# Optimization experiments

Hardware: AMD Instinct MI355X
Metric: run time of the kernel (lower is better)

Reference implementation:

```python
import jax, jax.numpy as jnp
import numpy as np

B, H, S, D = 4, 16, 2048, 64

def setup_inputs() -> dict:
    key = jax.random.key(0)
    kq, kk, kv = jax.random.split(key, 3)
    return {
        "query": jax.random.normal(kq, (B, H, S, D), dtype=jnp.float32),
        "key": jax.random.normal(kk, (B, H, S, D), dtype=jnp.float32),
        "value": jax.random.normal(kv, (B, H, S, D), dtype=jnp.float32),
        "dropout_p": 0,
    }

def reference(query, key, value, dropout_p):
    # qk: [B,H,S,S] materialized as in the original (unfused SDPA)
    scale = query.shape[-1] ** -0.5
    qk = jnp.einsum("bhqd,bhkd->bhqk", query, key) * scale
    attn = jax.nn.softmax(qk, axis=-1)
    # dropout_p == 0 -> identity (keeps reference deterministic)
    out = jnp.einsum("bhqk,bhkd->bhqd", attn, value)
    return out
```

## Files before the change

### kernel.cpp

```cpp
#include <hip/hip_runtime.h>
#include <hip/hip_bf16.h>

#define B_   4
#define H_   16
#define SEQ  2048
#define DH   64
#define BM   256
#define BN   64
#define NBH  (B_ * H_)
#define NELEM (NBH * SEQ * DH)

typedef __bf16 bf16x8 __attribute__((ext_vector_type(8)));
typedef float  f32x4  __attribute__((ext_vector_type(4)));
typedef unsigned short u16x8 __attribute__((ext_vector_type(8)));
typedef unsigned short u16x4 __attribute__((ext_vector_type(4)));

__device__ __forceinline__ unsigned short f2bu(float x) {
    __hip_bfloat16 h = __float2bfloat16(x);
    return __builtin_bit_cast(unsigned short, h);
}

__device__ __forceinline__ void ld_lds16(const unsigned short* g, unsigned short* l) {
    __builtin_amdgcn_global_load_lds(
        (const __attribute__((address_space(1))) unsigned int*)(g),
        (__attribute__((address_space(3))) unsigned int*)(l), 16, 0, 0);
}

__global__ __launch_bounds__(256)
void prep_kv(const float* __restrict__ K, const float* __restrict__ V,
             unsigned short* __restrict__ Kb, unsigned short* __restrict__ Vt) {
    __shared__ unsigned short tile[64 * 72];
    const int bh = blockIdx.y;
    const int s0 = blockIdx.x * 64;
    const int t  = threadIdx.x;

    {
        const float* Ki = K + (size_t)bh * SEQ * DH + (size_t)s0 * DH;
        unsigned short* Ko = Kb + (size_t)bh * SEQ * DH + (size_t)s0 * DH;
        for (int jj = 0; jj < 2; ++jj) {
            const int e = (jj * 256 + t) * 8;
            const float4 a = *reinterpret_cast<const float4*>(Ki + e);
            const float4 b = *reinterpret_cast<const float4*>(Ki + e + 4);
            u16x8 u;
            u[0] = f2bu(a.x); u[1] = f2bu(a.y); u[2] = f2bu(a.z); u[3] = f2bu(a.w);
            u[4] = f2bu(b.x); u[5] = f2bu(b.y); u[6] = f2bu(b.z); u[7] = f2bu(b.w);
            *reinterpret_cast<u16x8*>(Ko + e) = u;
        }
    }

    const float* Vb = V + (size_t)bh * SEQ * DH + (size_t)s0 * DH;
    unsigned short* Vo = Vt + (size_t)bh * DH * SEQ;
    {
        const int sl = t >> 2, d0 = (t & 3) * 16;
        for (int c = 0; c < 4; ++c) {
            const float4 v = *reinterpret_cast<const float4*>(Vb + sl * DH + d0 + c * 4);
            u16x4 u; u[0] = f2bu(v.x); u[1] = f2bu(v.y); u[2] = f2bu(v.z); u[3] = f2bu(v.w);
            *reinterpret_cast<u16x4*>(&tile[sl * 72 + d0 + c * 4]) = u;
        }
    }
    __syncthreads();
    {
        const int d = t >> 2, sc0 = (t & 3) * 16;
        for (int c = 0; c < 2; ++c) {
            const int s = sc0 + c * 8;
            u16x8 u;
#pragma unroll
            for (int r = 0; r < 8; ++r) u[r] = tile[(s + r) * 72 + d];
            *reinterpret_cast<u16x8*>(Vo + (size_t)d * SEQ + s0 + s) = u;
        }
    }
}

__global__ __launch_bounds__(256, 2)
void fa_fwd(const float* __restrict__ Qg, const unsigned short* __restrict__ Kb,
            const unsigned short* __restrict__ Vtb, float* __restrict__ Og)
{
    __shared__ __attribute__((aligned(16))) unsigned short smem[16384];

    const int tid  = threadIdx.x;
    const int lane = tid & 63;
    const int wave = tid >> 6;
    const int l15  = lane & 15;
    const int quad = lane >> 4;

    const int bid   = blockIdx.x;
    const int xcd   = bid & 7;
    const int jj    = bid >> 3;
    const int bh    = (xcd << 3) | (jj >> 3);
    const int qtile = jj & 7;

    const float*          Qb  = Qg  + (size_t)bh * SEQ * DH;
    const unsigned short* Kbh = Kb  + (size_t)bh * SEQ * DH;
    const unsigned short* Vbh = Vtb + (size_t)bh * DH * SEQ;
    float*                Ob  = Og  + (size_t)bh * SEQ * DH;

    const int qrow0 = qtile * BM + wave * 64;

    const float CS = 0.125f * 1.4426950408889634f;

    bf16x8 Qf[4][2];
#pragma unroll
    for (int rt = 0; rt < 4; ++rt) {
        const float* qsrc = Qb + (size_t)(qrow0 + rt * 16 + l15) * DH + quad * 8;
#pragma unroll
        for (int kt = 0; kt < 2; ++kt) {
            const float4 a = *reinterpret_cast<const float4*>(qsrc + kt * 32);
            const float4 b = *reinterpret_cast<const float4*>(qsrc + kt * 32 + 4);
            union { bf16x8 v; unsigned short u[8]; } tmp;
            tmp.u[0] = f2bu(a.x * CS); tmp.u[1] = f2bu(a.y * CS);
            tmp.u[2] = f2bu(a.z * CS); tmp.u[3] = f2bu(a.w * CS);
            tmp.u[4] = f2bu(b.x * CS); tmp.u[5] = f2bu(b.y * CS);
            tmp.u[6] = f2bu(b.z * CS); tmp.u[7] = f2bu(b.w * CS);
            Qf[rt][kt] = tmp.v;
        }
    }

    bf16x8 ones;
    {
        union { bf16x8 v; unsigned short u[8]; } t;
        for (int i = 0; i < 8; ++i) t.u[i] = 0x3F80;
        ones = t.v;
    }
    const f32x4 fzero = {0.f, 0.f, 0.f, 0.f};

    f32x4 Oacc[4][4];
    f32x4 Lacc[4];
#pragma unroll
    for (int rt = 0; rt < 4; ++rt) {
        Lacc[rt] = fzero;
#pragma unroll
        for (int dt = 0; dt < 4; ++dt) Oacc[rt][dt] = fzero;
    }

    const unsigned short* kp[2];
    const unsigned short* vp[2];
    int koff_st[2], voff_st[2];
    for (int i = 0; i < 2; ++i) {
        const int beta = i * 256 + tid;
        {
            const int s    = beta >> 3;
            const int b    = beta & 7;
            const int gnat = b ^ (s & 7);
            const int grow = 32 * (s >> 5) + 8 * ((s >> 2) & 3)
                           + 4 * ((s >> 4) & 1) + (s & 3);
            kp[i]  = Kbh + (size_t)grow * DH + gnat * 8;
        }
        {
            const int d = beta >> 3;
            const int g = (beta & 7) ^ (d & 7);
            vp[i]  = Vbh + (size_t)d * SEQ + g * 8;
        }
        koff_st[i] = (i * 256 + wave * 64) * 8;
        voff_st[i] = 4096 + (i * 256 + wave * 64) * 8;
    }

    const int sx   = l15 & 7;
    const int krd0 = l15 * 64 + ((quad    ) ^ sx) * 8;
    const int krd1 = l15 * 64 + ((quad + 4) ^ sx) * 8;
    const int vrd0 = l15 * 64 + ((quad    ) ^ sx) * 8;
    const int vrd1 = l15 * 64 + ((quad + 4) ^ sx) * 8;

#define STAGE(BUF) do {                                                        \
        _Pragma("unroll")                                                      \
        for (int i = 0; i < 2; ++i) {                                          \
            ld_lds16(kp[i], smem + (BUF) * 8192 + koff_st[i]);                 \
            kp[i] += BN * DH;                                                  \
        }                                                                      \
        _Pragma("unroll")                                                      \
        for (int i = 0; i < 2; ++i) {                                          \
            ld_lds16(vp[i], smem + (BUF) * 8192 + voff_st[i]);                 \
            vp[i] += BN;                                                       \
        }                                                                      \
    } while (0)

#define QK_PAIR(BUF, NT0, SACC) do {                                           \
        _Pragma("unroll")                                                      \
        for (int m = 0; m < 2; ++m) {                                          \
            const bf16x8 kf0 = *reinterpret_cast<const bf16x8*>(               \
                &smem[(BUF) * 8192 + ((NT0) + m) * 1024 + krd0]);              \
            const bf16x8 kf1 = *reinterpret_cast<const bf16x8*>(               \
                &smem[(BUF) * 8192 + ((NT0) + m) * 1024 + krd1]);              \
            _Pragma("unroll")                                                  \
            for (int rt = 0; rt < 4; ++rt) {                                   \
                SACC[rt][m] = __builtin_amdgcn_mfma_f32_16x16x32_bf16(kf0, Qf[rt][0], fzero,       0, 0, 0); \
                SACC[rt][m] = __builtin_amdgcn_mfma_f32_16x16x32_bf16(kf1, Qf[rt][1], SACC[rt][m], 0, 0, 0); \
            }                                                                  \
        }                                                                      \
    } while (0)

#define SM_HALF(SACC, KS) do {                                                 \
        _Pragma("unroll")                                                      \
        for (int rt = 0; rt < 4; ++rt) {                                       \
            union { bf16x8 v; unsigned w[4]; } a;                              \
            _Pragma("unroll")                                                  \
            for (int m = 0; m < 2; ++m) {                                      \
                _Pragma("unroll")                                              \
                for (int rp = 0; rp < 2; ++rp) {                               \
                    const float p0 = __builtin_amdgcn_exp2f(SACC[rt][m][2 * rp    ]); \
                    const float p1 = __builtin_amdgcn_exp2f(SACC[rt][m][2 * rp + 1]); \
                    const unsigned u0 = __builtin_bit_cast(unsigned, p0) + 0x8000u; \
                    const unsigned u1 = __builtin_bit_cast(unsigned, p1) + 0x8000u; \
                    a.w[m * 2 + rp] = __builtin_amdgcn_perm(u1, u0, 0x07060302u); \
                }                                                              \
            }                                                                  \
            af[rt][KS] = a.v;                                                  \
            Lacc[rt] = __builtin_amdgcn_mfma_f32_16x16x32_bf16(a.v, ones, Lacc[rt], 0, 0, 0); \
        }                                                                      \
    } while (0)

#define PV_HALF(BUF, KS, VRD) do {                                             \
        _Pragma("unroll")                                                      \
        for (int dt = 0; dt < 4; ++dt) {                                       \
            const bf16x8 bfr = *reinterpret_cast<const bf16x8*>(               \
                &smem[(BUF) * 8192 + 4096 + dt * 1024 + (VRD)]);               \
            _Pragma("unroll")                                                  \
            for (int rt = 0; rt < 4; ++rt)                                     \
                Oacc[rt][dt] = __builtin_amdgcn_mfma_f32_16x16x32_bf16(af[rt][KS], bfr, Oacc[rt][dt], 0, 0, 0); \
        }                                                                      \
    } while (0)

#define COMPUTE(BUF) do {                                                      \
        f32x4 SA[4][2], SB[4][2];                                              \
        bf16x8 af[4][2];                                                       \
        __builtin_amdgcn_s_setprio(1);                                         \
        QK_PAIR(BUF, 0, SA);                                                   \
        __builtin_amdgcn_s_setprio(0);                                         \
        SM_HALF(SA, 0);              \
        __builtin_amdgcn_s_setprio(1);                                         \
        QK_PAIR(BUF, 2, SB);                                                   \
        __builtin_amdgcn_s_setprio(0);                                         \
        SM_HALF(SB, 1);                                                        \
        __builtin_amdgcn_s_setprio(1);                                         \
        PV_HALF(BUF, 0, vrd0);                                                 \
        PV_HALF(BUF, 1, vrd1);                                                 \
        __builtin_amdgcn_s_setprio(0);                                         \
    } while (0)

    STAGE(0);
    __syncthreads();

#pragma unroll 1
    for (int it2 = 0; it2 < 15; ++it2) {
        STAGE(1);
        COMPUTE(0);
        __syncthreads();
        STAGE(0);
        COMPUTE(1);
        __syncthreads();
    }
    STAGE(1);
    COMPUTE(0);
    __syncthreads();
    COMPUTE(1);

#undef STAGE
#undef QK_PAIR
#undef SM_HALF
#undef PV_HALF
#undef COMPUTE

#pragma unroll
    for (int rt = 0; rt < 4; ++rt) {
#pragma unroll
        for (int r = 0; r < 4; ++r) {
            const float inv = 1.0f / Lacc[rt][r];
            const int row = qrow0 + rt * 16 + quad * 4 + r;
            float* orow = Ob + (size_t)row * DH + l15;
#pragma unroll
            for (int dt = 0; dt < 4; ++dt)
                orow[dt * 16] = Oacc[rt][dt][r] * inv;
        }
    }
}

extern "C" void kernel_launch(void* const* d_in, const int* in_sizes, int n_in,
                              void* d_out, int out_size, void* d_ws, size_t ws_size,
                              hipStream_t stream) {
    const float* Q = (const float*)d_in[0];
    const float* K = (const float*)d_in[1];
    const float* V = (const float*)d_in[2];
    float* O = (float*)d_out;

    unsigned short* Kb = (unsigned short*)d_ws;
    unsigned short* Vt = Kb + (size_t)NELEM;

    prep_kv<<<dim3(SEQ / 64, NBH), 256, 0, stream>>>(K, V, Kb, Vt);
    fa_fwd<<<dim3((SEQ / BM) * NBH), dim3(256), 0, stream>>>(Q, Kb, Vt, O);
}
```

Measured before the change: 199.3 us.

## Load K/V tiles straight into registers and halve the query tile

```diff
diff --git a/kernel.cpp b/kernel.cpp
--- a/kernel.cpp
+++ b/kernel.cpp
@@ -5,7 +5,7 @@
 #define H_   16
 #define SEQ  2048
 #define DH   64
-#define BM   256
+#define BM   128
 #define BN   64
 #define NBH  (B_ * H_)
 #define NELEM (NBH * SEQ * DH)
@@ -18,12 +18,6 @@
 __device__ __forceinline__ unsigned short f2bu(float x) {
     __hip_bfloat16 h = __float2bfloat16(x);
     return __builtin_bit_cast(unsigned short, h);
-}
-
-__device__ __forceinline__ void ld_lds16(const unsigned short* g, unsigned short* l) {
-    __builtin_amdgcn_global_load_lds(
-        (const __attribute__((address_space(1))) unsigned int*)(g),
-        (__attribute__((address_space(3))) unsigned int*)(l), 16, 0, 0);
 }
 
 __global__ __launch_bounds__(256)
@@ -75,8 +69,6 @@
 void fa_fwd(const float* __restrict__ Qg, const unsigned short* __restrict__ Kb,
             const unsigned short* __restrict__ Vtb, float* __restrict__ Og)
 {
-    __shared__ __attribute__((aligned(16))) unsigned short smem[16384];
-
     const int tid  = threadIdx.x;
     const int lane = tid & 63;
     const int wave = tid >> 6;
@@ -86,21 +78,21 @@
     const int bid   = blockIdx.x;
     const int xcd   = bid & 7;
     const int jj    = bid >> 3;
-    const int bh    = (xcd << 3) | (jj >> 3);
-    const int qtile = jj & 7;
+    const int bh    = (xcd << 3) | (jj >> 4);
+    const int qtile = jj & 15;
 
     const float*          Qb  = Qg  + (size_t)bh * SEQ * DH;
     const unsigned short* Kbh = Kb  + (size_t)bh * SEQ * DH;
     const unsigned short* Vbh = Vtb + (size_t)bh * DH * SEQ;
     float*                Ob  = Og  + (size_t)bh * SEQ * DH;
 
-    const int qrow0 = qtile * BM + wave * 64;
+    const int qrow0 = qtile * BM + wave * 32;
 
     const float CS = 0.125f * 1.4426950408889634f;
 
-    bf16x8 Qf[4][2];
-#pragma unroll
-    for (int rt = 0; rt < 4; ++rt) {
+    bf16x8 Qf[2][2];
+#pragma unroll
+    for (int rt = 0; rt < 2; ++rt) {
         const float* qsrc = Qb + (size_t)(qrow0 + rt * 16 + l15) * DH + quad * 8;
 #pragma unroll
         for (int kt = 0; kt < 2; ++kt) {
@@ -123,81 +115,73 @@
     }
     const f32x4 fzero = {0.f, 0.f, 0.f, 0.f};
 
-    f32x4 Oacc[4][4];
-    f32x4 Lacc[4];
-#pragma unroll
-    for (int rt = 0; rt < 4; ++rt) {
+    f32x4 Oacc[2][4];
+    f32x4 Lacc[2];
+#pragma unroll
+    for (int rt = 0; rt < 2; ++rt) {
         Lacc[rt] = fzero;
 #pragma unroll
         for (int dt = 0; dt < 4; ++dt) Oacc[rt][dt] = fzero;
     }
 
-    const unsigned short* kp[2];
-    const unsigned short* vp[2];
-    int koff_st[2], voff_st[2];
-    for (int i = 0; i < 2; ++i) {
-        const int beta = i * 256 + tid;
-        {
-            const int s    = beta >> 3;
-            const int b    = beta & 7;
-            const int gnat = b ^ (s & 7);
-            const int grow = 32 * (s >> 5) + 8 * ((s >> 2) & 3)
-                           + 4 * ((s >> 4) & 1) + (s & 3);
-            kp[i]  = Kbh + (size_t)grow * DH + gnat * 8;
-        }
-        {
-            const int d = beta >> 3;
-            const int g = (beta & 7) ^ (d & 7);
-            vp[i]  = Vbh + (size_t)d * SEQ + g * 8;
-        }
-        koff_st[i] = (i * 256 + wave * 64) * 8;
-        voff_st[i] = 4096 + (i * 256 + wave * 64) * 8;
-    }
-
-    const int sx   = l15 & 7;
-    const int krd0 = l15 * 64 + ((quad    ) ^ sx) * 8;
-    const int krd1 = l15 * 64 + ((quad + 4) ^ sx) * 8;
-    const int vrd0 = l15 * 64 + ((quad    ) ^ sx) * 8;
-    const int vrd1 = l15 * 64 + ((quad + 4) ^ sx) * 8;
-
-#define STAGE(BUF) do {                                                        \
-        _Pragma("unroll")                                                      \
-        for (int i = 0; i < 2; ++i) {                                          \
-            ld_lds16(kp[i], smem + (BUF) * 8192 + koff_st[i]);                 \
-            kp[i] += BN * DH;                                                  \
-        }                                                                      \
-        _Pragma("unroll")                                                      \
-        for (int i = 0; i < 2; ++i) {                                          \
-            ld_lds16(vp[i], smem + (BUF) * 8192 + voff_st[i]);                 \
-            vp[i] += BN;                                                       \
-        }                                                                      \
-    } while (0)
-
-#define QK_PAIR(BUF, NT0, SACC) do {                                           \
+    const int r15 = 8 * (l15 >> 2) + (l15 & 3);
+    int koff[8];
+#pragma unroll
+    for (int ks = 0; ks < 2; ++ks)
+#pragma unroll
+        for (int m = 0; m < 2; ++m)
+#pragma unroll
+            for (int kt = 0; kt < 2; ++kt)
+                koff[ks * 4 + m * 2 + kt] =
+                    (32 * ks + 4 * m + r15) * DH + quad * 8 + kt * 32;
+
+    int voff[8];
+#pragma unroll
+    for (int ks = 0; ks < 2; ++ks)
+#pragma unroll
+        for (int dt = 0; dt < 4; ++dt)
+            voff[ks * 4 + dt] = (dt * 16 + l15) * SEQ + ks * 32 + quad * 8;
+
+    const unsigned short* kbase = Kbh;
+    const unsigned short* vbase = Vbh;
+
+    bf16x8 KA[8], KB[8], Vf[8];
+
+#define KLOAD(DST, BASE) do {                                                  \
+        _Pragma("unroll")                                                      \
+        for (int x = 0; x < 8; ++x)                                            \
+            DST[x] = *reinterpret_cast<const bf16x8*>((BASE) + koff[x]);       \
+    } while (0)
+
+#define VLOAD(DST, BASE) do {                                                  \
+        _Pragma("unroll")                                                      \
+        for (int x = 0; x < 8; ++x)                                            \
+            DST[x] = *reinterpret_cast<const bf16x8*>((BASE) + voff[x]);       \
+    } while (0)
+
+#define QK_GRP(KSRC, KS, S) do {                                               \
         _Pragma("unroll")                                                      \
         for (int m = 0; m < 2; ++m) {                                          \
-            const bf16x8 kf0 = *reinterpret_cast<const bf16x8*>(               \
-                &smem[(BUF) * 8192 + ((NT0) + m) * 1024 + krd0]);              \
-            const bf16x8 kf1 = *reinterpret_cast<const bf16x8*>(               \
-                &smem[(BUF) * 8192 + ((NT0) + m) * 1024 + krd1]);              \
+            const bf16x8 kf0 = KSRC[(KS) * 4 + m * 2 + 0];                     \
+            const bf16x8 kf1 = KSRC[(KS) * 4 + m * 2 + 1];                     \
             _Pragma("unroll")                                                  \
-            for (int rt = 0; rt < 4; ++rt) {                                   \
-                SACC[rt][m] = __builtin_amdgcn_mfma_f32_16x16x32_bf16(kf0, Qf[rt][0], fzero,       0, 0, 0); \
-                SACC[rt][m] = __builtin_amdgcn_mfma_f32_16x16x32_bf16(kf1, Qf[rt][1], SACC[rt][m], 0, 0, 0); \
+            for (int rt = 0; rt < 2; ++rt) {                                   \
+                S[rt][m] = __builtin_amdgcn_mfma_f32_16x16x32_bf16(kf0, Qf[rt][0], fzero,    0, 0, 0); \
+                S[rt][m] = __builtin_amdgcn_mfma_f32_16x16x32_bf16(kf1, Qf[rt][1], S[rt][m], 0, 0, 0); \
             }                                                                  \
         }                                                                      \
     } while (0)
 
-#define SM_HALF(SACC, KS) do {                                                 \
-        _Pragma("unroll")                                                      \
-        for (int rt = 0; rt < 4; ++rt) {                                       \
+#define SM_GRP(S, KS) do {                                                     \
+        _Pragma("unroll")                                                      \
+        for (int rt = 0; rt < 2; ++rt) {                                       \
             union { bf16x8 v; unsigned w[4]; } a;                              \
             _Pragma("unroll")                                                  \
             for (int m = 0; m < 2; ++m) {                                      \
                 _Pragma("unroll")                                              \
                 for (int rp = 0; rp < 2; ++rp) {                               \
-                    const float p0 = __builtin_amdgcn_exp2f(SACC[rt][m][2 * rp    ]); \
-                    const float p1 = __builtin_amdgcn_exp2f(SACC[rt][m][2 * rp + 1]); \
+                    const float p0 = __builtin_amdgcn_exp2f(S[rt][m][2 * rp    ]); \
+                    const float p1 = __builtin_amdgcn_exp2f(S[rt][m][2 * rp + 1]); \
                     const unsigned u0 = __builtin_bit_cast(unsigned, p0) + 0x8000u; \
                     const unsigned u1 = __builtin_bit_cast(unsigned, p1) + 0x8000u; \
                     a.w[m * 2 + rp] = __builtin_amdgcn_perm(u1, u0, 0x07060302u); \
@@ -208,59 +192,56 @@
         }                                                                      \
     } while (0)
 
-#define PV_HALF(BUF, KS, VRD) do {                                             \
+#define PV_GRP(VSRC, KS) do {                                                  \
         _Pragma("unroll")                                                      \
         for (int dt = 0; dt < 4; ++dt) {                                       \
-            const bf16x8 bfr = *reinterpret_cast<const bf16x8*>(               \
-                &smem[(BUF) * 8192 + 4096 + dt * 1024 + (VRD)]);               \
+            const bf16x8 bfr = VSRC[(KS) * 4 + dt];                            \
             _Pragma("unroll")                                                  \
-            for (int rt = 0; rt < 4; ++rt)                                     \
+            for (int rt = 0; rt < 2; ++rt)                                     \
                 Oacc[rt][dt] = __builtin_amdgcn_mfma_f32_16x16x32_bf16(af[rt][KS], bfr, Oacc[rt][dt], 0, 0, 0); \
         }                                                                      \
     } while (0)
 
-#define COMPUTE(BUF) do {                                                      \
-        f32x4 SA[4][2], SB[4][2];                                              \
-        bf16x8 af[4][2];                                                       \
+#define COMPUTE(KSRC, VSRC) do {                                               \
+        f32x4 S[2][2];                                                         \
+        bf16x8 af[2][2];                                                       \
         __builtin_amdgcn_s_setprio(1);                                         \
-        QK_PAIR(BUF, 0, SA);                                                   \
+        QK_GRP(KSRC, 0, S);                                                    \
         __builtin_amdgcn_s_setprio(0);                                         \
-        SM_HALF(SA, 0);              \
+        SM_GRP(S, 0);                                                          \
         __builtin_amdgcn_s_setprio(1);                                         \
-        QK_PAIR(BUF, 2, SB);                                                   \
+        QK_GRP(KSRC, 1, S);                                                    \
         __builtin_amdgcn_s_setprio(0);                                         \
-        SM_HALF(SB, 1);                                                        \
+        SM_GRP(S, 1);                                                          \
         __builtin_amdgcn_s_setprio(1);                                         \
-        PV_HALF(BUF, 0, vrd0);                                                 \
-        PV_HALF(BUF, 1, vrd1);                                                 \
+        PV_GRP(VSRC, 0);                                                       \
+        PV_GRP(VSRC, 1);                                                       \
         __builtin_amdgcn_s_setprio(0);                                         \
     } while (0)
 
-    STAGE(0);
-    __syncthreads();
+    KLOAD(KA, kbase); kbase += BN * DH;
 
 #pragma unroll 1
-    for (int it2 = 0; it2 < 15; ++it2) {
-        STAGE(1);
-        COMPUTE(0);
-        __syncthreads();
-        STAGE(0);
-        COMPUTE(1);
-        __syncthreads();
-    }
-    STAGE(1);
-    COMPUTE(0);
-    __syncthreads();
-    COMPUTE(1);
-
-#undef STAGE
-#undef QK_PAIR
-#undef SM_HALF
-#undef PV_HALF
+    for (int it2 = 0; it2 < 16; ++it2) {
+        VLOAD(Vf, vbase);
+        KLOAD(KB, kbase); kbase += BN * DH;
+        COMPUTE(KA, Vf);
+        vbase += BN;
+        VLOAD(Vf, vbase);
+        KLOAD(KA, kbase); kbase += BN * DH;
+        COMPUTE(KB, Vf);
+        vbase += BN;
+    }
+
+#undef KLOAD
+#undef VLOAD
+#undef QK_GRP
+#undef SM_GRP
+#undef PV_GRP
 #undef COMPUTE
 
 #pragma unroll
-    for (int rt = 0; rt < 4; ++rt) {
+    for (int rt = 0; rt < 2; ++rt) {
 #pragma unroll
         for (int r = 0; r < 4; ++r) {
             const float inv = 1.0f / Lacc[rt][r];
```

Measured after the change: 358.7 us. 1.8x slower.
